# Kernel tuning notes

Measured on AMD Instinct MI355X. Metric: run time of the kernel, lower is better.

Reference implementation:

```python
import jax, jax.numpy as jnp
import numpy as np

D_MODEL = 1024
N_HEADS = 16
HEAD_DIM = D_MODEL // N_HEADS
D_FF = 4096
LN_EPS = 1e-5


def _layer_norm(x, gamma, beta):
    mu = jnp.mean(x, axis=-1, keepdims=True)
    var = jnp.var(x, axis=-1, keepdims=True)
    return (x - mu) * jax.lax.rsqrt(var + LN_EPS) * gamma + beta


def setup_inputs() -> dict:
    key = jax.random.key(0)
    ks = jax.random.split(key, 16)
    s = 1.0 / np.sqrt(D_MODEL)
    sf = 1.0 / np.sqrt(D_FF)
    return {
        "x": jax.random.normal(ks[0], (4, 2048, D_MODEL), dtype=jnp.float32),
        "w_q": jax.random.uniform(ks[1], (D_MODEL, D_MODEL), jnp.float32, -s, s),
        "b_q": jax.random.uniform(ks[2], (D_MODEL,), jnp.float32, -s, s),
        "w_k": jax.random.uniform(ks[3], (D_MODEL, D_MODEL), jnp.float32, -s, s),
        "b_k": jax.random.uniform(ks[4], (D_MODEL,), jnp.float32, -s, s),
        "w_v": jax.random.uniform(ks[5], (D_MODEL, D_MODEL), jnp.float32, -s, s),
        "b_v": jax.random.uniform(ks[6], (D_MODEL,), jnp.float32, -s, s),
        "w_o": jax.random.uniform(ks[7], (D_MODEL, D_MODEL), jnp.float32, -s, s),
        "b_o": jax.random.uniform(ks[8], (D_MODEL,), jnp.float32, -s, s),
        "ln1_g": jnp.ones((D_MODEL,), jnp.float32),
        "ln1_b": jnp.zeros((D_MODEL,), jnp.float32),
        "w1": jax.random.uniform(ks[9], (D_MODEL, D_FF), jnp.float32, -s, s),
        "b1": jax.random.uniform(ks[10], (D_FF,), jnp.float32, -s, s),
        "w2": jax.random.uniform(ks[11], (D_FF, D_MODEL), jnp.float32, -sf, sf),
        "b2": jax.random.uniform(ks[12], (D_MODEL,), jnp.float32, -sf, sf),
        "ln2_g": jnp.ones((D_MODEL,), jnp.float32),
        "ln2_b": jnp.zeros((D_MODEL,), jnp.float32),
    }


def reference(x, w_q, b_q, w_k, b_k, w_v, b_v, w_o, b_o,
              ln1_g, ln1_b, w1, b1, w2, b2, ln2_g, ln2_b):
    B, S, D = x.shape
    # projections -> [B, H, S, Hd]
    def split_heads(t):
        return t.reshape(B, S, N_HEADS, HEAD_DIM).transpose(0, 2, 1, 3)
    q = split_heads(x @ w_q + b_q)
    k = split_heads(x @ w_k + b_k)
    v = split_heads(x @ w_v + b_v)
    scale = jnp.float32(np.sqrt(HEAD_DIM))
    scores = jnp.einsum('bhqd,bhkd->bhqk', q, k) / scale
    attn = jax.nn.softmax(scores, axis=-1)  # dropout = identity in eval
    ctx = jnp.einsum('bhqk,bhkd->bhqd', attn, v)
    ctx = ctx.transpose(0, 2, 1, 3).reshape(B, S, D)
    attn_out = ctx @ w_o + b_o
    h = _layer_norm(x + attn_out, ln1_g, ln1_b)
    ffn = jax.nn.relu(h @ w1 + b1) @ w2 + b2
    return _layer_norm(h + ffn, ln2_g, ln2_b)
```

## Files before the change

### kernel.cpp

```cpp
#include <hip/hip_runtime.h>
#include <cstdint>
#include <cstddef>

typedef unsigned short u16;
typedef short s16x8 __attribute__((ext_vector_type(8)));
typedef unsigned short u16x8 __attribute__((ext_vector_type(8)));
typedef unsigned short u16x4 __attribute__((ext_vector_type(4)));
typedef float f32x4 __attribute__((ext_vector_type(4)));

#define MFMA_BF16(a, b, c) __builtin_amdgcn_mfma_f32_16x16x32_bf16((a), (b), (c), 0, 0, 0)

__device__ __forceinline__ float b2f(u16 u) {
    union { unsigned int i; float f; } x;
    x.i = ((unsigned int)u) << 16;
    return x.f;
}
__device__ __forceinline__ u16 f2b(float f) {
    union { float f; unsigned int i; } x;
    x.f = f;
    return (u16)((x.i + 0x8000u) >> 16);
}
__device__ __forceinline__ float exp2_hw(float x) {
    float r;
    asm volatile("v_exp_f32 %0, %1" : "=v"(r) : "v"(x));
    return r;
}

__device__ __forceinline__ void gload_lds16(const u16* g, u16* l) {
    __builtin_amdgcn_global_load_lds((__attribute__((address_space(1))) void*)(g),
                                     (__attribute__((address_space(3))) void*)(l),
                                     16, 0, 0);
}

__device__ __forceinline__ void transpose_tile(const float* __restrict__ in,
                                               u16* __restrict__ out,
                                               int R, int C, int bx, int by) {
    __shared__ u16 t[64][68];
    const int tc = bx * 64, tr = by * 64;
    for (int i = 0; i < 16; i++) {
        int idx = threadIdx.x + i * 256;
        int r = idx >> 6, c = idx & 63;
        t[r][c] = f2b(in[(size_t)(tr + r) * C + tc + c]);
    }
    __syncthreads();
    for (int i = 0; i < 16; i++) {
        int idx = threadIdx.x + i * 256;
        int r = idx >> 6, c = idx & 63;
        out[(size_t)(tc + r) * R + tr + c] = t[c][r];
    }
}

__global__ __launch_bounds__(256)
void prep_all(const float* __restrict__ w_q, const float* __restrict__ w_k,
              const float* __restrict__ w_v, const float* __restrict__ w_o,
              const float* __restrict__ w1, const float* __restrict__ w2,
              const float* __restrict__ x,
              u16* __restrict__ wqkv_t, u16* __restrict__ wo_t,
              u16* __restrict__ w1_t, u16* __restrict__ w2_t,
              u16* __restrict__ x_bf) {
    const int id = blockIdx.x;
    if (id < 1024) {
        const int j = id >> 8, lid = id & 255;
        const float* in = (j == 0) ? w_q : (j == 1) ? w_k : (j == 2) ? w_v : w_o;
        u16* out = (j == 0) ? wqkv_t
                 : (j == 1) ? wqkv_t + 1024 * 1024
                 : (j == 2) ? wqkv_t + 2 * 1024 * 1024
                 : wo_t;
        transpose_tile(in, out, 1024, 1024, lid & 15, lid >> 4);
    } else if (id < 2048) {
        const int lid = id - 1024;
        transpose_tile(w1, w1_t, 1024, 4096, lid & 63, lid >> 6);
    } else if (id < 3072) {
        const int lid = id - 2048;
        transpose_tile(w2, w2_t, 4096, 1024, lid & 15, lid >> 4);
    } else {
        const int i = ((id - 3072) * 256 + threadIdx.x) * 8;
        float4 a = *(const float4*)(x + i);
        float4 b = *(const float4*)(x + i + 4);
        u16x8 o;
        o[0] = f2b(a.x); o[1] = f2b(a.y); o[2] = f2b(a.z); o[3] = f2b(a.w);
        o[4] = f2b(b.x); o[5] = f2b(b.y); o[6] = f2b(b.z); o[7] = f2b(b.w);
        *(u16x8*)(x_bf + i) = o;
    }
}

enum { EPI_PLAIN = 0, EPI_RELU = 1, EPI_QKV = 2 };
#define SC_QK 0.1803368801111204f

template <int EPI>
__global__ __launch_bounds__(256, 3)
void gemm_bt(const u16* __restrict__ A, const u16* __restrict__ Bt,
             const float* __restrict__ bias0, const float* __restrict__ bias1,
             const float* __restrict__ bias2,
             u16* __restrict__ C0, u16* __restrict__ C1, u16* __restrict__ C2,
             int M, int N, int K) {
    __shared__ u16 As[128 * 64];
    __shared__ u16 Bs[128 * 64];
    const int tid = threadIdx.x;
    const int lane = tid & 63;
    const int wave = tid >> 6;
    const int qd = lane >> 4, cl = lane & 15;
    const int wr = (wave >> 1) * 64, wc = (wave & 1) * 64;
    const int m0 = blockIdx.x * 128, n0 = blockIdx.y * 128;

    const u16* AgP[4];
    const u16* BgP[4];
    int dsto[4];
    for (int c = 0; c < 4; c++) {
        const int d = tid * 8 + c * 2048;
        const int row = d >> 6;
        const int sblk = ((d >> 3) & 7) ^ (row & 7);
        AgP[c] = A + (size_t)(m0 + row) * K + sblk * 8;
        BgP[c] = Bt + (size_t)(n0 + row) * K + sblk * 8;
        dsto[c] = d;
    }

    const f32x4 Z = {0.f, 0.f, 0.f, 0.f};
    f32x4 acc[4][4];
    for (int i = 0; i < 4; i++)
        for (int j = 0; j < 4; j++) acc[i][j] = Z;

    for (int k = 0; k < K; k += 64) {
        __syncthreads();
        for (int c = 0; c < 4; c++) {
            gload_lds16(AgP[c] + k, As + dsto[c]);
            gload_lds16(BgP[c] + k, Bs + dsto[c]);
        }
        __syncthreads();
        for (int kk = 0; kk < 2; kk++) {
            s16x8 af[4], bfr[4];
            for (int i = 0; i < 4; i++) {
                const int row = wr + i * 16 + cl;
                af[i] = *(const s16x8*)(As + row * 64 +
                                        (((kk << 2) | qd) ^ (row & 7)) * 8);
            }
            for (int j = 0; j < 4; j++) {
                const int row = wc + j * 16 + cl;
                bfr[j] = *(const s16x8*)(Bs + row * 64 +
                                         (((kk << 2) | qd) ^ (row & 7)) * 8);
            }
            for (int i = 0; i < 4; i++)
                for (int j = 0; j < 4; j++)
                    acc[i][j] = MFMA_BF16(af[i], bfr[j], acc[i][j]);
        }
    }

    for (int j = 0; j < 4; j++) {
        const int col = n0 + wc + j * 16 + cl;
        float bv;
        if (EPI == EPI_QKV) {
            const int t = col >> 10, nn = col & 1023;
            const float* bp = (t == 0) ? bias0 : ((t == 1) ? bias1 : bias2);
            bv = bp[nn];
        } else {
            bv = bias0[col];
        }
        if (EPI == EPI_QKV && (col >> 10) == 2) {
            const int nn = col & 1023;
            const int hh = nn >> 6, d = nn & 63;
            for (int i = 0; i < 4; i++) {
                const int row0 = m0 + wr + i * 16 + qd * 4;
                const int b = row0 >> 11, s = row0 & 2047;
                const int bh = b * 16 + hh;
                u16x4 pk;
                for (int r = 0; r < 4; r++) pk[r] = f2b(acc[i][j][r] + bv);
                *(u16x4*)(&C2[((size_t)bh * 64 + d) * 2048 + s]) = pk;
            }
        } else {
            for (int i = 0; i < 4; i++) {
                for (int r = 0; r < 4; r++) {
                    const int row = m0 + wr + i * 16 + qd * 4 + r;
                    float v = acc[i][j][r] + bv;
                    if (EPI == EPI_RELU) v = fmaxf(v, 0.f);
                    if (EPI == EPI_QKV) {
                        const int t = col >> 10, nn = col & 1023;
                        const int hh = nn >> 6, d = nn & 63;
                        const int b = row >> 11, s = row & 2047;
                        const int bh = b * 16 + hh;
                        if (t == 0)
                            C0[((size_t)bh * 2048 + s) * 64 + d] = f2b(v * SC_QK);
                        else
                            C1[((size_t)bh * 2048 + s) * 64 + d] = f2b(v);
                    } else {
                        C0[(size_t)row * N + col] = f2b(v);
                    }
                }
            }
        }
    }
}

__global__ __launch_bounds__(256)
void flash_attn(const u16* __restrict__ Q, const u16* __restrict__ K,
                const u16* __restrict__ Vt, u16* __restrict__ ctx) {
    __shared__ u16 Ks[64 * 64];
    __shared__ u16 Vs[64 * 64];
    __shared__ u16 Ps[4][32 * 72];
    const int tid = threadIdx.x, lane = tid & 63, wave = tid >> 6;
    const int qd = lane >> 4, cl = lane & 15;
    const int bh = blockIdx.x;
    const int s0 = blockIdx.y * 128 + wave * 32;

    const u16* Qb = Q + ((size_t)bh * 2048 + s0) * 64;
    s16x8 qf[2][2];
    for (int m = 0; m < 2; m++) {
        qf[m][0] = *(const s16x8*)(Qb + (m * 16 + cl) * 64 + qd * 8);
        qf[m][1] = *(const s16x8*)(Qb + (m * 16 + cl) * 64 + 32 + qd * 8);
    }

    const f32x4 Z = {0.f, 0.f, 0.f, 0.f};
    f32x4 o_acc[2][4], l_lane[2];
    for (int m = 0; m < 2; m++) {
        l_lane[m] = Z;
        for (int t = 0; t < 4; t++) o_acc[m][t] = Z;
    }

    const u16* Kb = K + (size_t)bh * 2048 * 64;
    const u16* Vb = Vt + (size_t)bh * 64 * 2048;

    const int e0 = tid, e1 = tid + 256;
    const int r0 = e0 >> 3, bb0 = (e0 & 7) ^ (r0 & 7);
    const int r1 = e1 >> 3, bb1 = (e1 & 7) ^ (r1 & 7);
    u16* pw = &Ps[wave][0];

    for (int kb = 0; kb < 32; kb++) {
        __syncthreads();
        gload_lds16(Kb + (size_t)(kb * 64 + r0) * 64 + bb0 * 8, Ks + e0 * 8);
        gload_lds16(Kb + (size_t)(kb * 64 + r1) * 64 + bb1 * 8, Ks + e1 * 8);
        gload_lds16(Vb + (size_t)r0 * 2048 + kb * 64 + bb0 * 8, Vs + e0 * 8);
        gload_lds16(Vb + (size_t)r1 * 2048 + kb * 64 + bb1 * 8, Vs + e1 * 8);
        __syncthreads();

        f32x4 sacc[2][4];
        for (int m = 0; m < 2; m++)
            for (int t = 0; t < 4; t++) sacc[m][t] = Z;
        for (int t = 0; t < 4; t++) {
            const int row = t * 16 + cl;
            s16x8 kf0 = *(const s16x8*)(Ks + row * 64 + (qd ^ (row & 7)) * 8);
            s16x8 kf1 = *(const s16x8*)(Ks + row * 64 + ((qd + 4) ^ (row & 7)) * 8);
            for (int m = 0; m < 2; m++) {
                sacc[m][t] = MFMA_BF16(qf[m][0], kf0, sacc[m][t]);
                sacc[m][t] = MFMA_BF16(qf[m][1], kf1, sacc[m][t]);
            }
        }

        for (int m = 0; m < 2; m++)
            for (int t = 0; t < 4; t++) {
                f32x4 p;
                for (int r = 0; r < 4; r++) p[r] = exp2_hw(sacc[m][t][r]);
                l_lane[m] += p;
                for (int r = 0; r < 4; r++)
                    pw[(m * 16 + qd * 4 + r) * 72 + t * 16 + cl] = f2b(p[r]);
            }

        for (int kk = 0; kk < 2; kk++) {
            s16x8 vf[4];
            for (int t = 0; t < 4; t++) {
                const int row = t * 16 + cl;
                vf[t] = *(const s16x8*)(Vs + row * 64 +
                                        ((kk * 4 + qd) ^ (row & 7)) * 8);
            }
            for (int m = 0; m < 2; m++) {
                s16x8 pf = *(const s16x8*)(pw + (m * 16 + cl) * 72 + kk * 32 + qd * 8);
                for (int t = 0; t < 4; t++)
                    o_acc[m][t] = MFMA_BF16(pf, vf[t], o_acc[m][t]);
            }
        }
    }

    const int b = bh >> 4, hh = bh & 15;
    for (int m = 0; m < 2; m++)
        for (int r = 0; r < 4; r++) {
            float l = l_lane[m][r];
            for (int off = 1; off < 16; off <<= 1)
                l += __shfl_xor(l, off, 16);
            const float inv = 1.f / l;
            const int s = s0 + m * 16 + qd * 4 + r;
            for (int t = 0; t < 4; t++)
                ctx[((size_t)(b * 2048 + s)) * 1024 + hh * 64 + t * 16 + cl] =
                    f2b(o_acc[m][t][r] * inv);
        }
}

template <int MODE>
__global__ __launch_bounds__(256)
void ln_res(const void* __restrict__ Xv, const u16* __restrict__ Y,
            const float* __restrict__ G, const float* __restrict__ Bp,
            void* __restrict__ Ov) {
    const int row = blockIdx.x * 4 + (threadIdx.x >> 6);
    const int lane = threadIdx.x & 63;
    const int off = lane * 16;
    float v[16];
    float s = 0.f, s2 = 0.f;
    const u16* y = Y + (size_t)row * 1024 + off;
    if (MODE == 0) {
        const float* X = (const float*)Xv + (size_t)row * 1024 + off;
        for (int i = 0; i < 2; i++) {
            float4 xa = *(const float4*)(X + i * 8);
            float4 xb = *(const float4*)(X + i * 8 + 4);
            u16x8 yv = *(const u16x8*)(y + i * 8);
            float xs[8] = {xa.x, xa.y, xa.z, xa.w, xb.x, xb.y, xb.z, xb.w};
            for (int j = 0; j < 8; j++) {
                const float t = xs[j] + b2f(yv[j]);
                v[i * 8 + j] = t;
                s += t;
                s2 += t * t;
            }
        }
    } else {
        const u16* X = (const u16*)Xv + (size_t)row * 1024 + off;
        for (int i = 0; i < 2; i++) {
            u16x8 xv = *(const u16x8*)(X + i * 8);
            u16x8 yv = *(const u16x8*)(y + i * 8);
            for (int j = 0; j < 8; j++) {
                const float t = b2f(xv[j]) + b2f(yv[j]);
                v[i * 8 + j] = t;
                s += t;
                s2 += t * t;
            }
        }
    }
    for (int o = 32; o >= 1; o >>= 1) {
        s += __shfl_xor(s, o, 64);
        s2 += __shfl_xor(s2, o, 64);
    }
    const float mu = s * (1.f / 1024.f);
    const float var = s2 * (1.f / 1024.f) - mu * mu;
    const float rs = rsqrtf(var + 1e-5f);
    const float* g = G + off;
    const float* bp = Bp + off;
    for (int i = 0; i < 2; i++) {
        float4 ga = *(const float4*)(g + i * 8);
        float4 gb = *(const float4*)(g + i * 8 + 4);
        float4 ba = *(const float4*)(bp + i * 8);
        float4 bb = *(const float4*)(bp + i * 8 + 4);
        float gs[8] = {ga.x, ga.y, ga.z, ga.w, gb.x, gb.y, gb.z, gb.w};
        float bs[8] = {ba.x, ba.y, ba.z, ba.w, bb.x, bb.y, bb.z, bb.w};
        if (MODE == 0) {
            u16* o = (u16*)Ov + (size_t)row * 1024 + off;
            u16x8 ov;
            for (int j = 0; j < 8; j++)
                ov[j] = f2b((v[i * 8 + j] - mu) * rs * gs[j] + bs[j]);
            *(u16x8*)(o + i * 8) = ov;
        } else {
            float* o = (float*)Ov + (size_t)row * 1024 + off;
            float4 o0, o1;
            o0.x = (v[i * 8 + 0] - mu) * rs * gs[0] + bs[0];
            o0.y = (v[i * 8 + 1] - mu) * rs * gs[1] + bs[1];
            o0.z = (v[i * 8 + 2] - mu) * rs * gs[2] + bs[2];
            o0.w = (v[i * 8 + 3] - mu) * rs * gs[3] + bs[3];
            o1.x = (v[i * 8 + 4] - mu) * rs * gs[4] + bs[4];
            o1.y = (v[i * 8 + 5] - mu) * rs * gs[5] + bs[5];
            o1.z = (v[i * 8 + 6] - mu) * rs * gs[6] + bs[6];
            o1.w = (v[i * 8 + 7] - mu) * rs * gs[7] + bs[7];
            *(float4*)(o + i * 8) = o0;
            *(float4*)(o + i * 8 + 4) = o1;
        }
    }
}

extern "C" void kernel_launch(void* const* d_in, const int* in_sizes, int n_in,
                              void* d_out, int out_size, void* d_ws, size_t ws_size,
                              hipStream_t stream) {
    const float* x    = (const float*)d_in[0];
    const float* w_q  = (const float*)d_in[1];
    const float* b_q  = (const float*)d_in[2];
    const float* w_k  = (const float*)d_in[3];
    const float* b_k  = (const float*)d_in[4];
    const float* w_v  = (const float*)d_in[5];
    const float* b_v  = (const float*)d_in[6];
    const float* w_o  = (const float*)d_in[7];
    const float* b_o  = (const float*)d_in[8];
    const float* ln1g = (const float*)d_in[9];
    const float* ln1b = (const float*)d_in[10];
    const float* w1   = (const float*)d_in[11];
    const float* b1   = (const float*)d_in[12];
    const float* w2   = (const float*)d_in[13];
    const float* b2   = (const float*)d_in[14];
    const float* ln2g = (const float*)d_in[15];
    const float* ln2b = (const float*)d_in[16];
    float* out = (float*)d_out;

    char* ws = (char*)d_ws;
    const size_t MB = 1024 * 1024;
    u16* wqkv_t = (u16*)(ws + 0);
    u16* wo_t   = (u16*)(ws + 6 * MB);
    u16* w1_t   = (u16*)(ws + 8 * MB);
    u16* w2_t   = (u16*)(ws + 16 * MB);
    u16* x_bf   = (u16*)(ws + 24 * MB);
    u16* Qs     = (u16*)(ws + 40 * MB);
    u16* Kk     = (u16*)(ws + 56 * MB);
    u16* Vt     = (u16*)(ws + 72 * MB);
    u16* ctx    = (u16*)(ws + 88 * MB);
    u16* attn   = (u16*)(ws + 104 * MB);
    u16* h      = attn;
    u16* ffn1   = (u16*)(ws + 24 * MB);
    u16* ffn2   = (u16*)(ws + 88 * MB);

    prep_all<<<7168, 256, 0, stream>>>(w_q, w_k, w_v, w_o, w1, w2, x,
                                       wqkv_t, wo_t, w1_t, w2_t, x_bf);

    gemm_bt<EPI_QKV><<<dim3(64, 24), 256, 0, stream>>>(
        x_bf, wqkv_t, b_q, b_k, b_v, Qs, Kk, Vt, 8192, 3072, 1024);

    flash_attn<<<dim3(64, 16), 256, 0, stream>>>(Qs, Kk, Vt, ctx);

    gemm_bt<EPI_PLAIN><<<dim3(64, 8), 256, 0, stream>>>(
        ctx, wo_t, b_o, nullptr, nullptr, attn, nullptr, nullptr, 8192, 1024, 1024);

    ln_res<0><<<2048, 256, 0, stream>>>(x, attn, ln1g, ln1b, h);

    gemm_bt<EPI_RELU><<<dim3(64, 32), 256, 0, stream>>>(
        h, w1_t, b1, nullptr, nullptr, ffn1, nullptr, nullptr, 8192, 4096, 1024);
    gemm_bt<EPI_PLAIN><<<dim3(64, 8), 256, 0, stream>>>(
        ffn1, w2_t, b2, nullptr, nullptr, ffn2, nullptr, nullptr, 8192, 1024, 4096);

    ln_res<1><<<2048, 256, 0, stream>>>(h, ffn2, ln2g, ln2b, out);

    (void)in_sizes; (void)n_in; (void)out_size; (void)ws_size;
}
```

Before: 519.1 us.

## Double-buffer K/V tiles in flash attention and compute row sums via MFMA

The flash attention kernel now keeps two LDS buffers for the K and V tiles. It issues the next tile's global-to-LDS loads before computing on the current tile, and needs only one barrier per iteration instead of two. The softmax denominator is now built by an extra MFMA of P against a vector of bf16 ones, which replaces the per-lane VALU adds and the cross-lane shuffle reduction at the end. This doubles K/V LDS use and adds a few MFMAs per tile. The row sum now uses bf16-rounded probabilities, which matches the values used in the PV product.

```diff
diff --git a/kernel.cpp b/kernel.cpp
--- a/kernel.cpp
+++ b/kernel.cpp
@@ -193,14 +193,26 @@
 __global__ __launch_bounds__(256)
 void flash_attn(const u16* __restrict__ Q, const u16* __restrict__ K,
                 const u16* __restrict__ Vt, u16* __restrict__ ctx) {
-    __shared__ u16 Ks[64 * 64];
-    __shared__ u16 Vs[64 * 64];
+    __shared__ u16 Ks[2][64 * 64];
+    __shared__ u16 Vs[2][64 * 64];
     __shared__ u16 Ps[4][32 * 72];
     const int tid = threadIdx.x, lane = tid & 63, wave = tid >> 6;
     const int qd = lane >> 4, cl = lane & 15;
     const int bh = blockIdx.x;
     const int s0 = blockIdx.y * 128 + wave * 32;
 
+    const u16* Kb = K + (size_t)bh * 2048 * 64;
+    const u16* Vb = Vt + (size_t)bh * 64 * 2048;
+
+    const int e0 = tid, e1 = tid + 256;
+    const int r0 = e0 >> 3, bb0 = (e0 & 7) ^ (r0 & 7);
+    const int r1 = e1 >> 3, bb1 = (e1 & 7) ^ (r1 & 7);
+
+    gload_lds16(Kb + (size_t)r0 * 64 + bb0 * 8, &Ks[0][e0 * 8]);
+    gload_lds16(Kb + (size_t)r1 * 64 + bb1 * 8, &Ks[0][e1 * 8]);
+    gload_lds16(Vb + (size_t)r0 * 2048 + bb0 * 8, &Vs[0][e0 * 8]);
+    gload_lds16(Vb + (size_t)r1 * 2048 + bb1 * 8, &Vs[0][e1 * 8]);
+
     const u16* Qb = Q + ((size_t)bh * 2048 + s0) * 64;
     s16x8 qf[2][2];
     for (int m = 0; m < 2; m++) {
@@ -208,36 +220,38 @@
         qf[m][1] = *(const s16x8*)(Qb + (m * 16 + cl) * 64 + 32 + qd * 8);
     }
 
+    s16x8 onesf;
+    for (int i = 0; i < 8; i++) onesf[i] = (short)0x3F80;
+
     const f32x4 Z = {0.f, 0.f, 0.f, 0.f};
-    f32x4 o_acc[2][4], l_lane[2];
+    f32x4 o_acc[2][4], l_acc[2];
     for (int m = 0; m < 2; m++) {
-        l_lane[m] = Z;
+        l_acc[m] = Z;
         for (int t = 0; t < 4; t++) o_acc[m][t] = Z;
     }
 
-    const u16* Kb = K + (size_t)bh * 2048 * 64;
-    const u16* Vb = Vt + (size_t)bh * 64 * 2048;
-
-    const int e0 = tid, e1 = tid + 256;
-    const int r0 = e0 >> 3, bb0 = (e0 & 7) ^ (r0 & 7);
-    const int r1 = e1 >> 3, bb1 = (e1 & 7) ^ (r1 & 7);
     u16* pw = &Ps[wave][0];
+    __syncthreads();
 
     for (int kb = 0; kb < 32; kb++) {
-        __syncthreads();
-        gload_lds16(Kb + (size_t)(kb * 64 + r0) * 64 + bb0 * 8, Ks + e0 * 8);
-        gload_lds16(Kb + (size_t)(kb * 64 + r1) * 64 + bb1 * 8, Ks + e1 * 8);
-        gload_lds16(Vb + (size_t)r0 * 2048 + kb * 64 + bb0 * 8, Vs + e0 * 8);
-        gload_lds16(Vb + (size_t)r1 * 2048 + kb * 64 + bb1 * 8, Vs + e1 * 8);
-        __syncthreads();
+        const int cur = kb & 1;
+        if (kb < 31) {
+            const int kn = kb + 1;
+            gload_lds16(Kb + (size_t)(kn * 64 + r0) * 64 + bb0 * 8, &Ks[cur ^ 1][e0 * 8]);
+            gload_lds16(Kb + (size_t)(kn * 64 + r1) * 64 + bb1 * 8, &Ks[cur ^ 1][e1 * 8]);
+            gload_lds16(Vb + (size_t)r0 * 2048 + kn * 64 + bb0 * 8, &Vs[cur ^ 1][e0 * 8]);
+            gload_lds16(Vb + (size_t)r1 * 2048 + kn * 64 + bb1 * 8, &Vs[cur ^ 1][e1 * 8]);
+        }
+        const u16* ks = Ks[cur];
+        const u16* vs = Vs[cur];
 
         f32x4 sacc[2][4];
         for (int m = 0; m < 2; m++)
             for (int t = 0; t < 4; t++) sacc[m][t] = Z;
         for (int t = 0; t < 4; t++) {
             const int row = t * 16 + cl;
-            s16x8 kf0 = *(const s16x8*)(Ks + row * 64 + (qd ^ (row & 7)) * 8);
-            s16x8 kf1 = *(const s16x8*)(Ks + row * 64 + ((qd + 4) ^ (row & 7)) * 8);
+            s16x8 kf0 = *(const s16x8*)(ks + row * 64 + (qd ^ (row & 7)) * 8);
+            s16x8 kf1 = *(const s16x8*)(ks + row * 64 + ((qd + 4) ^ (row & 7)) * 8);
             for (int m = 0; m < 2; m++) {
                 sacc[m][t] = MFMA_BF16(qf[m][0], kf0, sacc[m][t]);
                 sacc[m][t] = MFMA_BF16(qf[m][1], kf1, sacc[m][t]);
@@ -248,7 +262,6 @@
             for (int t = 0; t < 4; t++) {
                 f32x4 p;
                 for (int r = 0; r < 4; r++) p[r] = exp2_hw(sacc[m][t][r]);
-                l_lane[m] += p;
                 for (int r = 0; r < 4; r++)
                     pw[(m * 16 + qd * 4 + r) * 72 + t * 16 + cl] = f2b(p[r]);
             }
@@ -257,24 +270,23 @@
             s16x8 vf[4];
             for (int t = 0; t < 4; t++) {
                 const int row = t * 16 + cl;
-                vf[t] = *(const s16x8*)(Vs + row * 64 +
+                vf[t] = *(const s16x8*)(vs + row * 64 +
                                         ((kk * 4 + qd) ^ (row & 7)) * 8);
             }
             for (int m = 0; m < 2; m++) {
                 s16x8 pf = *(const s16x8*)(pw + (m * 16 + cl) * 72 + kk * 32 + qd * 8);
                 for (int t = 0; t < 4; t++)
                     o_acc[m][t] = MFMA_BF16(pf, vf[t], o_acc[m][t]);
-            }
-        }
+                l_acc[m] = MFMA_BF16(pf, onesf, l_acc[m]);
+            }
+        }
+        __syncthreads();
     }
 
     const int b = bh >> 4, hh = bh & 15;
     for (int m = 0; m < 2; m++)
         for (int r = 0; r < 4; r++) {
-            float l = l_lane[m][r];
-            for (int off = 1; off < 16; off <<= 1)
-                l += __shfl_xor(l, off, 16);
-            const float inv = 1.f / l;
+            const float inv = 1.f / l_acc[m][r];
             const int s = s0 + m * 16 + qd * 4 + r;
             for (int t = 0; t < 4; t++)
                 ctx[((size_t)(b * 2048 + s)) * 1024 + hh * 64 + t * 16 + cl] =
```

Result: no change. 523.3 us (+0.8%).
